# Performance work log

Measured on AMD Instinct MI355X. Metric: run time of the kernel, lower is better.

Reference implementation:

```python
import jax, jax.numpy as jnp
import numpy as np

N_KNOTS = 16
DEGREE = 3
EPS = 1e-8


def make_knots(n_knots, degree):
    knots = np.zeros(n_knots, dtype=np.float32)
    for i in range(n_knots):
        if i <= degree:
            knots[i] = 0.0
        elif i >= n_knots - degree - 1:
            knots[i] = 1.0
        else:
            knots[i] = (i - degree) / (n_knots - 2 * degree - 1)
    return knots


def setup_inputs() -> dict:
    key = jax.random.key(0)
    k1, k2 = jax.random.split(key)
    x = jax.random.uniform(k1, (65536, 64), dtype=jnp.float32)
    control_points = jax.random.normal(k2, (64, 12, 64), dtype=jnp.float32)
    return {"x": x, "control_points": control_points}


def bspline_basis(x, knots_np, degree):
    # x: [B, D] in [0,1]; returns basis: [B, D, n_control_points]
    n_knots = knots_np.shape[0]
    n_intervals = n_knots - 1
    knots = jnp.asarray(knots_np)
    xe = x[..., None]  # [B, D, 1]
    left = knots[:-1]
    right = knots[1:]
    in_interval = (xe >= left) & (xe < right)
    last = (xe >= left[-1]) & (xe <= right[-1])  # include right endpoint of last interval
    basis = jnp.concatenate([in_interval[..., :-1], last], axis=-1).astype(x.dtype)
    for k in range(1, degree + 1):
        nb = n_intervals - k
        j = np.arange(nb)
        dL = knots_np[j + k] - knots_np[j]          # constants
        dR = knots_np[j + k + 1] - knots_np[j + 1]
        okL = np.abs(dL) > EPS
        okR = np.abs(dR) > EPS
        invL = jnp.asarray(np.where(okL, 1.0 / np.where(okL, dL, 1.0), 0.0).astype(np.float32))
        invR = jnp.asarray(np.where(okR, 1.0 / np.where(okR, dR, 1.0), 0.0).astype(np.float32))
        cL = (xe - knots[j]) * invL                 # [B, D, nb], zero where degenerate
        cR = (knots[j + k + 1] - xe) * invR
        basis = cL * basis[..., :nb] + cR * basis[..., 1:nb + 1]
    return basis


def reference(x, control_points):
    # x: [B, in_dim]; control_points: [in_dim, n_cp, out_dim]
    knots_np = make_knots(N_KNOTS, DEGREE)
    xc = jnp.clip(x, 0.0, 1.0)
    basis = bspline_basis(xc, knots_np, DEGREE)     # [B, in_dim, n_cp]
    return jnp.einsum('bic,ico->bo', basis, control_points)
```

## Files before the change

kernel.cpp:

```cpp
#include <hip/hip_runtime.h>


typedef short short8 __attribute__((ext_vector_type(8)));
typedef float f32x4 __attribute__((ext_vector_type(4)));
typedef unsigned u32x4 __attribute__((ext_vector_type(4)));

#define NFEAT 64
#define NSTEP 24
#define CHUNK 16
#define CHUNKS 8
#define RPB   (CHUNK*CHUNKS)
#define THREADS 256
#define RDW   387

static __device__ __forceinline__ unsigned bf16rne(float f) {
  unsigned u = __float_as_uint(f);
  return (u + 0x7FFFu + ((u >> 16) & 1u)) >> 16;
}

__global__ __launch_bounds__(256) void prep_wfrag(const float* __restrict__ cp,
                                                  unsigned* __restrict__ wfrag) {
  int id = blockIdx.x * 256 + threadIdx.x;
  int d  = id & 3;
  int l  = (id >> 2) & 63;
  int id2 = id >> 8;
  int nt = id2 / NSTEP;
  int s  = id2 - nt * NSTEP;
  int g  = l >> 4;
  int o  = nt * 16 + (l & 15);
  int e0 = 2 * d;
  int k0 = s * 32 + ((e0 < 4) ? (4 * g + e0) : (16 + 4 * g + (e0 - 4)));
  unsigned lo = bf16rne(cp[k0 * 64 + o]);
  unsigned hi = bf16rne(cp[(k0 + 1) * 64 + o]);
  wfrag[id] = lo | (hi << 16);
}

static __device__ __forceinline__ void eval_pack(float xi, unsigned* __restrict__ dst) {
  xi = fminf(fmaxf(xi, 0.0f), 1.0f);
  float t9 = xi * 9.0f;
  int jj = (int)t9;
  float validf = (jj <= 8) ? 1.0f : 0.0f;
  jj = (jj > 8) ? 8 : jj;
  float fj = (float)jj;
  float u  = t9 - fj;
  float omu = 1.0f - u;
  float c1  = fminf(fj, 1.0f);
  float c2  = fminf(fj, 2.0f);
  float rdj = 9.0f - fj;
  float d2p = fminf(rdj, 2.0f);
  float d3p = fminf(rdj, 3.0f);
  float invA = (jj == 0) ? 1.0f : 0.5f;
  float invB = (jj == 8) ? 1.0f : 0.5f;
  float invC = (jj == 0) ? 1.0f : ((jj == 1) ? 0.5f : (1.0f/3.0f));
  float invD = (jj == 0 || jj == 8) ? 0.5f : (1.0f/3.0f);
  float invE = (jj >= 7) ? ((jj == 8) ? 1.0f : 0.5f) : (1.0f/3.0f);
  float xkm1 = u + c1, xkm2 = u + c2;
  float k2x = d2p - u, k3x = d3p - u;
  float t0 = omu * invA;
  float A0 = omu * t0;
  float s1 = xkm1 * t0;
  float t1 = u * invB;
  float A1 = fmaf(k2x, t1, s1);
  float A2 = u * t1;
  float u0 = A0 * invC;
  float B0 = omu * u0;
  float s2 = xkm2 * u0;
  float u1 = A1 * invD;
  float B1 = fmaf(k2x, u1, s2);
  float s3 = xkm1 * u1;
  float u2 = A2 * invE;
  float B2 = fmaf(k3x, u2, s3);
  float B3 = u * u2;
  B0 *= validf; B1 *= validf; B2 *= validf; B3 *= validf;

  unsigned b0 = bf16rne(B0), b1 = bf16rne(B1), b2 = bf16rne(B2), b3 = bf16rne(B3);
  unsigned p01 = b0 | (b1 << 16);
  unsigned p23 = b2 | (b3 << 16);
  unsigned O0 = p01 << 16;
  unsigned O1 = (p01 >> 16) | (p23 << 16);
  unsigned O2 = p23 >> 16;
  int e2 = jj >> 1;
  bool odd = (jj & 1) != 0;
  #pragma unroll
  for (int q = 0; q < 6; ++q) {
    unsigned ve = (q == e2) ? p01 : ((q == e2 + 1) ? p23 : 0u);
    unsigned vo = (q == e2) ? O0 : ((q == e2 + 1) ? O1 : ((q == e2 + 2) ? O2 : 0u));
    dst[q] = odd ? vo : ve;
  }
}

__global__ __launch_bounds__(THREADS) void kan_mfma(const float* __restrict__ x,
                                                    const unsigned* __restrict__ wfrag,
                                                    float* __restrict__ out) {
  __shared__ unsigned bsd[2][CHUNK * RDW];
  const int tid  = threadIdx.x;
  const int lane = tid & 63;
  const int w    = tid >> 6;
  const long rowBase = (long)blockIdx.x * RPB;

  short8 bfr[NSTEP];
  {
    const short8* wp = (const short8*)wfrag + (w * NSTEP * 64 + lane);
    #pragma unroll
    for (int s = 0; s < NSTEP; ++s) bfr[s] = wp[s * 64];
  }

  const int br  = tid >> 4;
  const int bi0 = (tid & 15) * 4;
  const int m = lane & 15, g = lane >> 4;

  {
    const float4 xv = *(const float4*)(x + (rowBase + br) * 64 + bi0);
    float xs4[4] = {xv.x, xv.y, xv.z, xv.w};
    #pragma unroll
    for (int e = 0; e < 4; ++e)
      eval_pack(xs4[e], &bsd[0][br * RDW + (bi0 + e) * 6]);
  }
  __syncthreads();

  for (int c = 0; c < CHUNKS; ++c) {
    const int cur = c & 1;

    float xs4[4];
    if (c < CHUNKS - 1) {
      const float4 xv = *(const float4*)(x + (rowBase + (c + 1) * CHUNK + br) * 64 + bi0);
      xs4[0] = xv.x; xs4[1] = xv.y; xs4[2] = xv.z; xs4[3] = xv.w;
    }

    f32x4 acc = {0.0f, 0.0f, 0.0f, 0.0f};
    {
      const short* base = (const short*)&bsd[cur][0] + m * (2 * RDW) + g * 4;
      #pragma unroll
      for (int s = 0; s < NSTEP; ++s) {
        const unsigned* pa = (const unsigned*)(base + s * 32);
        const unsigned* pb = (const unsigned*)(base + s * 32 + 16);
        u32x4 q = { pa[0], pa[1], pb[0], pb[1] };
        acc = __builtin_amdgcn_mfma_f32_16x16x32_bf16(
            __builtin_bit_cast(short8, q), bfr[s], acc, 0, 0, 0);
      }
    }
    {
      float* op = out + (rowBase + c * CHUNK + g * 4) * 64 + w * 16 + m;
      #pragma unroll
      for (int j = 0; j < 4; ++j) op[j * 64] = acc[j];
    }

    if (c < CHUNKS - 1) {
      #pragma unroll
      for (int e = 0; e < 4; ++e)
        eval_pack(xs4[e], &bsd[cur ^ 1][br * RDW + (bi0 + e) * 6]);
    }
    __syncthreads();
  }
}

extern "C" void kernel_launch(void* const* d_in, const int* in_sizes, int n_in,
                              void* d_out, int out_size, void* d_ws, size_t ws_size,
                              hipStream_t stream) {
  const float* x  = (const float*)d_in[0];
  const float* cp = (const float*)d_in[1];
  float* out = (float*)d_out;
  unsigned* wfrag = (unsigned*)d_ws;

  hipLaunchKernelGGL(prep_wfrag, dim3(96), dim3(256), 0, stream, cp, wfrag);
  const int rows = in_sizes[0] / NFEAT;
  hipLaunchKernelGGL(kan_mfma, dim3(rows / RPB), dim3(THREADS), 0, stream,
                     x, wfrag, out);
}
```

Baseline: 90.61 us.

## Build A fragments in registers and stage weights in LDS per wave

Restructures the MFMA kernel so each wave evaluates B-spline bases for its own 32 rows directly into A-operand registers, removing the shared-memory basis round trip and per-chunk barriers. The K dimension is reordered so each lane's basis words line up with MFMA fragments, and prep_wfrag is rewritten to match. Weight fragments now live in LDS, staged in two halves and shared by 8 waves, instead of being held in per-wave registers. Each wave computes a 32x64 output tile with 8 accumulators, which trades higher register pressure and LDS reads of B for less LDS traffic and synchronization on A.

Result: no change. 91.87 us (+1.4%).

```diff
diff --git a/kernel.cpp b/kernel.cpp
--- a/kernel.cpp
+++ b/kernel.cpp
@@ -5,13 +5,12 @@
 typedef float f32x4 __attribute__((ext_vector_type(4)));
 typedef unsigned u32x4 __attribute__((ext_vector_type(4)));
 
-#define NFEAT 64
 #define NSTEP 24
-#define CHUNK 16
-#define CHUNKS 8
-#define RPB   (CHUNK*CHUNKS)
-#define THREADS 256
-#define RDW   387
+#define HSTEP 12
+#define WAVES 8
+#define THREADS (WAVES * 64)
+#define RPW 32
+#define RPB (WAVES * RPW)
 
 static __device__ __forceinline__ unsigned bf16rne(float f) {
   unsigned u = __float_as_uint(f);
@@ -24,18 +23,22 @@
   int d  = id & 3;
   int l  = (id >> 2) & 63;
   int id2 = id >> 8;
-  int nt = id2 / NSTEP;
-  int s  = id2 - nt * NSTEP;
-  int g  = l >> 4;
-  int o  = nt * 16 + (l & 15);
-  int e0 = 2 * d;
-  int k0 = s * 32 + ((e0 < 4) ? (4 * g + e0) : (16 + 4 * g + (e0 - 4)));
+  int p   = id2 / 48;
+  int rem = id2 - p * 48;
+  int nt  = rem / 12;
+  int sl  = rem - nt * 12;
+  int s   = p * 12 + sl;
+  int g   = l >> 4;
+  int o   = nt * 16 + (l & 15);
+  int k0  = 192 * g + 8 * s + 2 * d;
   unsigned lo = bf16rne(cp[k0 * 64 + o]);
   unsigned hi = bf16rne(cp[(k0 + 1) * 64 + o]);
   wfrag[id] = lo | (hi << 16);
 }
 
-static __device__ __forceinline__ void eval_pack(float xi, unsigned* __restrict__ dst) {
+struct Pack6 { unsigned w0, w1, w2, w3, w4, w5; };
+
+static __device__ __forceinline__ Pack6 eval_pack(float xi) {
   xi = fminf(fmaxf(xi, 0.0f), 1.0f);
   float t9 = xi * 9.0f;
   int jj = (int)t9;
@@ -51,9 +54,9 @@
   float d3p = fminf(rdj, 3.0f);
   float invA = (jj == 0) ? 1.0f : 0.5f;
   float invB = (jj == 8) ? 1.0f : 0.5f;
-  float invC = (jj == 0) ? 1.0f : ((jj == 1) ? 0.5f : (1.0f/3.0f));
-  float invD = (jj == 0 || jj == 8) ? 0.5f : (1.0f/3.0f);
-  float invE = (jj >= 7) ? ((jj == 8) ? 1.0f : 0.5f) : (1.0f/3.0f);
+  float invC = (jj == 0) ? 1.0f : ((jj == 1) ? 0.5f : (1.0f / 3.0f));
+  float invD = (jj == 0 || jj == 8) ? 0.5f : (1.0f / 3.0f);
+  float invE = (jj >= 7) ? ((jj == 8) ? 1.0f : 0.5f) : (1.0f / 3.0f);
   float xkm1 = u + c1, xkm2 = u + c2;
   float k2x = d2p - u, k3x = d3p - u;
   float t0 = omu * invA;
@@ -81,77 +84,104 @@
   unsigned O2 = p23 >> 16;
   int e2 = jj >> 1;
   bool odd = (jj & 1) != 0;
-  #pragma unroll
-  for (int q = 0; q < 6; ++q) {
-    unsigned ve = (q == e2) ? p01 : ((q == e2 + 1) ? p23 : 0u);
-    unsigned vo = (q == e2) ? O0 : ((q == e2 + 1) ? O1 : ((q == e2 + 2) ? O2 : 0u));
-    dst[q] = odd ? vo : ve;
-  }
+#define VE(q) ((q == e2) ? p01 : ((q == e2 + 1) ? p23 : 0u))
+#define VO(q) ((q == e2) ? O0 : ((q == e2 + 1) ? O1 : ((q == e2 + 2) ? O2 : 0u)))
+  Pack6 r;
+  r.w0 = odd ? VO(0) : VE(0);
+  r.w1 = odd ? VO(1) : VE(1);
+  r.w2 = odd ? VO(2) : VE(2);
+  r.w3 = odd ? VO(3) : VE(3);
+  r.w4 = odd ? VO(4) : VE(4);
+  r.w5 = odd ? VO(5) : VE(5);
+#undef VE
+#undef VO
+  return r;
 }
 
 __global__ __launch_bounds__(THREADS) void kan_mfma(const float* __restrict__ x,
                                                     const unsigned* __restrict__ wfrag,
                                                     float* __restrict__ out) {
-  __shared__ unsigned bsd[2][CHUNK * RDW];
+  __shared__ u32x4 ldsB[4 * HSTEP * 64];
   const int tid  = threadIdx.x;
   const int lane = tid & 63;
   const int w    = tid >> 6;
-  const long rowBase = (long)blockIdx.x * RPB;
+  const int m = lane & 15, g = lane >> 4;
+  const long row0 = ((long)blockIdx.x * WAVES + w) * RPW;
 
-  short8 bfr[NSTEP];
+  float xr0[16], xr1[16];
   {
-    const short8* wp = (const short8*)wfrag + (w * NSTEP * 64 + lane);
+    const float4* p0 = (const float4*)(x + (row0 + m) * 64 + g * 16);
+    const float4* p1 = (const float4*)(x + (row0 + 16 + m) * 64 + g * 16);
     #pragma unroll
-    for (int s = 0; s < NSTEP; ++s) bfr[s] = wp[s * 64];
+    for (int q = 0; q < 4; ++q) {
+      float4 v = p0[q];
+      xr0[4 * q] = v.x; xr0[4 * q + 1] = v.y; xr0[4 * q + 2] = v.z; xr0[4 * q + 3] = v.w;
+    }
+    #pragma unroll
+    for (int q = 0; q < 4; ++q) {
+      float4 v = p1[q];
+      xr1[4 * q] = v.x; xr1[4 * q + 1] = v.y; xr1[4 * q + 2] = v.z; xr1[4 * q + 3] = v.w;
+    }
   }
 
-  const int br  = tid >> 4;
-  const int bi0 = (tid & 15) * 4;
-  const int m = lane & 15, g = lane >> 4;
+  f32x4 acc[2][4];
+  #pragma unroll
+  for (int mt = 0; mt < 2; ++mt)
+    #pragma unroll
+    for (int nt = 0; nt < 4; ++nt)
+      acc[mt][nt] = f32x4{0.0f, 0.0f, 0.0f, 0.0f};
 
-  {
-    const float4 xv = *(const float4*)(x + (rowBase + br) * 64 + bi0);
-    float xs4[4] = {xv.x, xv.y, xv.z, xv.w};
+  const u32x4* wsrc = (const u32x4*)wfrag;
+
+  #pragma unroll
+  for (int p = 0; p < 2; ++p) {
+    if (p) __syncthreads();
     #pragma unroll
-    for (int e = 0; e < 4; ++e)
-      eval_pack(xs4[e], &bsd[0][br * RDW + (bi0 + e) * 6]);
-  }
-  __syncthreads();
+    for (int q = 0; q < (4 * HSTEP * 64) / THREADS; ++q)
+      ldsB[q * THREADS + tid] = wsrc[p * 3072 + q * THREADS + tid];
+    __syncthreads();
 
-  for (int c = 0; c < CHUNKS; ++c) {
-    const int cur = c & 1;
-
-    float xs4[4];
-    if (c < CHUNKS - 1) {
-      const float4 xv = *(const float4*)(x + (rowBase + (c + 1) * CHUNK + br) * 64 + bi0);
-      xs4[0] = xv.x; xs4[1] = xv.y; xs4[2] = xv.z; xs4[3] = xv.w;
-    }
-
-    f32x4 acc = {0.0f, 0.0f, 0.0f, 0.0f};
-    {
-      const short* base = (const short*)&bsd[cur][0] + m * (2 * RDW) + g * 4;
+    #pragma unroll
+    for (int tl = 0; tl < 4; ++tl) {
+      const int t = p * 4 + tl;
+      Pack6 aA = eval_pack(xr0[2 * t]);
+      Pack6 aB = eval_pack(xr0[2 * t + 1]);
+      Pack6 bA = eval_pack(xr1[2 * t]);
+      Pack6 bB = eval_pack(xr1[2 * t + 1]);
       #pragma unroll
-      for (int s = 0; s < NSTEP; ++s) {
-        const unsigned* pa = (const unsigned*)(base + s * 32);
-        const unsigned* pb = (const unsigned*)(base + s * 32 + 16);
-        u32x4 q = { pa[0], pa[1], pb[0], pb[1] };
-        acc = __builtin_amdgcn_mfma_f32_16x16x32_bf16(
-            __builtin_bit_cast(short8, q), bfr[s], acc, 0, 0, 0);
+      for (int sub = 0; sub < 3; ++sub) {
+        u32x4 qa, qb;
+        if (sub == 0) {
+          qa[0] = aA.w0; qa[1] = aA.w1; qa[2] = aA.w2; qa[3] = aA.w3;
+          qb[0] = bA.w0; qb[1] = bA.w1; qb[2] = bA.w2; qb[3] = bA.w3;
+        } else if (sub == 1) {
+          qa[0] = aA.w4; qa[1] = aA.w5; qa[2] = aB.w0; qa[3] = aB.w1;
+          qb[0] = bA.w4; qb[1] = bA.w5; qb[2] = bB.w0; qb[3] = bB.w1;
+        } else {
+          qa[0] = aB.w2; qa[1] = aB.w3; qa[2] = aB.w4; qa[3] = aB.w5;
+          qb[0] = bB.w2; qb[1] = bB.w3; qb[2] = bB.w4; qb[3] = bB.w5;
+        }
+        short8 A0 = __builtin_bit_cast(short8, qa);
+        short8 A1 = __builtin_bit_cast(short8, qb);
+        const int sl = 3 * tl + sub;
+        #pragma unroll
+        for (int nt = 0; nt < 4; ++nt) {
+          u32x4 bq = ldsB[(nt * HSTEP + sl) * 64 + lane];
+          short8 B = __builtin_bit_cast(short8, bq);
+          acc[0][nt] = __builtin_amdgcn_mfma_f32_16x16x32_bf16(A0, B, acc[0][nt], 0, 0, 0);
+          acc[1][nt] = __builtin_amdgcn_mfma_f32_16x16x32_bf16(A1, B, acc[1][nt], 0, 0, 0);
+        }
       }
     }
-    {
-      float* op = out + (rowBase + c * CHUNK + g * 4) * 64 + w * 16 + m;
+  }
+
+  #pragma unroll
+  for (int mt = 0; mt < 2; ++mt)
+    #pragma unroll
+    for (int nt = 0; nt < 4; ++nt)
       #pragma unroll
-      for (int j = 0; j < 4; ++j) op[j * 64] = acc[j];
-    }
-
-    if (c < CHUNKS - 1) {
-      #pragma unroll
-      for (int e = 0; e < 4; ++e)
-        eval_pack(xs4[e], &bsd[cur ^ 1][br * RDW + (bi0 + e) * 6]);
-    }
-    __syncthreads();
-  }
+      for (int j = 0; j < 4; ++j)
+        out[(row0 + mt * 16 + g * 4 + j) * 64 + nt * 16 + m] = acc[mt][nt][j];
 }
 
 extern "C" void kernel_launch(void* const* d_in, const int* in_sizes, int n_in,
@@ -163,7 +193,7 @@
   unsigned* wfrag = (unsigned*)d_ws;
 
   hipLaunchKernelGGL(prep_wfrag, dim3(96), dim3(256), 0, stream, cp, wfrag);
-  const int rows = in_sizes[0] / NFEAT;
+  const int rows = in_sizes[0] / 64;
   hipLaunchKernelGGL(kan_mfma, dim3(rows / RPB), dim3(THREADS), 0, stream,
                      x, wfrag, out);
 }
```
